# Optimization experiments

Hardware: AMD Instinct MI355X
Metric: run time of the kernel (lower is better)

The kernel has to match this reference:

```python
import jax, jax.numpy as jnp
import numpy as np

T, B, I, H = 1024, 256, 128, 256

def setup_inputs() -> dict:
    key = jax.random.key(0)
    k1, k2, k3, k4, k5 = jax.random.split(key, 5)
    x = jax.random.normal(k1, (T, B, I), dtype=jnp.float32)
    # nn.Linear default init: U(-1/sqrt(fan_in), 1/sqrt(fan_in))
    sW = 1.0 / np.sqrt(I)
    sV = 1.0 / np.sqrt(H)
    W = jax.random.uniform(k2, (H, I), minval=-sW, maxval=sW, dtype=jnp.float32)
    b_W = jax.random.uniform(k3, (H,), minval=-sW, maxval=sW, dtype=jnp.float32)
    V = jax.random.uniform(k4, (H, H), minval=-sV, maxval=sV, dtype=jnp.float32)
    b_V = jax.random.uniform(k5, (H,), minval=-sV, maxval=sV, dtype=jnp.float32)
    return {"x": x, "W": W, "b_W": b_W, "V": V, "b_V": b_V}

def reference(x, W, b_W, V, b_V):
    # x: (T, B, I). Hidden is always initialized to zeros (as in the torch code).
    # Precompute input projection for all timesteps (same math, one big GEMM).
    xW = jnp.einsum('tbi,hi->tbh', x, W) + b_W  # (T, B, H)
    h0 = jnp.zeros((x.shape[1], V.shape[0]), dtype=x.dtype)

    def step(h, xw_t):
        h_new = jnp.tanh(xw_t + h @ V.T + b_V)
        return h_new, h_new

    h_final, h_seq = jax.lax.scan(step, h0, xW)
    return h_seq, h_final
```

## Files before the change

### kernel.cpp

```cpp
#include <hip/hip_runtime.h>
#include <hip/hip_fp16.h>

#define TT 1024
#define BB 256
#define II 128
#define HH 256

typedef _Float16 f16x8 __attribute__((ext_vector_type(8)));
typedef _Float16 h2    __attribute__((ext_vector_type(2)));
typedef float    f32x4 __attribute__((ext_vector_type(4)));

union HU { h2 h; unsigned u; };
static __device__ __forceinline__ h2 as_h2(unsigned v) { HU t; t.u = v; return t.h; }
static __device__ __forceinline__ unsigned pack2f(float a, float b)
{
    HU t; t.h = h2{(_Float16)a, (_Float16)b}; return t.u;
}
static __device__ __forceinline__ float fdot2u(unsigned a, unsigned b, float c)
{
    return __builtin_amdgcn_fdot2(as_h2(a), as_h2(b), c, false);
}

#define LDS_BARRIER()                                            \
    do {                                                         \
        asm volatile("s_waitcnt lgkmcnt(0)" ::: "memory");       \
        __builtin_amdgcn_s_barrier();                            \
        __builtin_amdgcn_sched_barrier(0);                       \
    } while (0)

__device__ __forceinline__ float fast_tanh(float a)
{
    float e = __builtin_amdgcn_exp2f(a * 2.8853900817779268f);
    return 1.0f - 2.0f * __builtin_amdgcn_rcpf(e + 1.0f);
}

static __device__ __forceinline__ f16x8 cvt8(const float* p)
{
    float4 a = *(const float4*)p;
    float4 b = *(const float4*)(p + 4);
    f16x8 r;
    r[0]=(_Float16)a.x; r[1]=(_Float16)a.y; r[2]=(_Float16)a.z; r[3]=(_Float16)a.w;
    r[4]=(_Float16)b.x; r[5]=(_Float16)b.y; r[6]=(_Float16)b.z; r[7]=(_Float16)b.w;
    return r;
}

__global__ __launch_bounds__(256, 1)
void xw_gemm(const float* __restrict__ x, const float* __restrict__ W,
             const float* __restrict__ bW, const float* __restrict__ bV,
             float* __restrict__ xw)
{
    __shared__ _Float16 Wl[HH * II];
    const int tid  = threadIdx.x;
    const int l    = tid & 63;
    const int wv   = (__builtin_amdgcn_readfirstlane(tid) >> 6) & 3;
    const int lr   = l & 15;
    const int kgrp = l >> 4;

    {
        const int row = tid;
        const float4* src = (const float4*)(W + (size_t)row * II);
        unsigned* dst = (unsigned*)Wl;
        const int sw = (row & 7) << 4;
#pragma unroll
        for (int q = 0; q < II / 4; ++q) {
            float4 v = src[q];
            dst[(row * 256 + ((q * 8) ^ sw)) >> 2]     = pack2f(v.x, v.y);
            dst[(row * 256 + ((q * 8 + 4) ^ sw)) >> 2] = pack2f(v.z, v.w);
        }
    }
    __syncthreads();

    const size_t Mbase = (size_t)blockIdx.x * 64;
    const size_t arow  = Mbase + 16 * wv + lr;

    f16x8 afr[4];
#pragma unroll
    for (int kc = 0; kc < 4; ++kc)
        afr[kc] = cvt8(x + arow * II + kc * 32 + kgrp * 8);

    f32x4 acc[16];
#pragma unroll
    for (int nt = 0; nt < 16; ++nt) acc[nt] = f32x4{0.f, 0.f, 0.f, 0.f};

#pragma unroll
    for (int nt = 0; nt < 16; ++nt) {
        const int col = nt * 16 + lr;
        const int sw  = (col & 7) << 4;
#pragma unroll
        for (int kc = 0; kc < 4; ++kc) {
            f16x8 bfr = *(const f16x8*)((const char*)Wl + col * 256 +
                                        ((kc * 64 + kgrp * 16) ^ sw));
            acc[nt] = __builtin_amdgcn_mfma_f32_16x16x32_f16(afr[kc], bfr, acc[nt], 0, 0, 0);
        }
    }
#pragma unroll
    for (int nt = 0; nt < 16; ++nt) {
        const float bias = bW[nt * 16 + lr] + bV[nt * 16 + lr];
#pragma unroll
        for (int r = 0; r < 4; ++r) {
            size_t row = Mbase + 16 * wv + kgrp * 4 + r;
            xw[row * HH + nt * 16 + lr] = acc[nt][r] + bias;
        }
    }
}

__global__ __launch_bounds__(512, 2)
void rnn_v(const float* __restrict__ V, float* __restrict__ out)
{
    const int b   = blockIdx.x;
    const int tid = threadIdx.x;
    const int l   = tid & 63;
    const int w   = (__builtin_amdgcn_readfirstlane(tid) >> 6) & 7;
    const int lb  = 8 * w;

    __shared__ __align__(16) _Float16 hbuf[2][HH];
    __shared__ __align__(16) float    pbuf[8][HH];

    unsigned Vreg[4][16];
#pragma unroll
    for (int c = 0; c < 4; ++c) {
        const int j = 4 * l + c;
        const float* vr = V + (size_t)j * HH + 32 * w;
#pragma unroll
        for (int m = 0; m < 16; ++m) Vreg[c][m] = pack2f(vr[2 * m], vr[2 * m + 1]);
    }

    if (tid < HH) { hbuf[0][tid] = (_Float16)0.f; hbuf[1][tid] = (_Float16)0.f; }
    __syncthreads();

    float* __restrict__ seq = out;
    float* __restrict__ fin = out + (size_t)TT * BB * HH;

    float XA = 0.f, XB = 0.f;
    if (tid < HH) {
        XA = seq[((size_t)0 * BB + b) * HH + tid];
        XB = seq[((size_t)1 * BB + b) * HH + tid];
    }

#define RSTEP(P, X, T)                                                          \
    {                                                                           \
        uint2 hv = *(const uint2*)&hbuf[P][4 * l];             \
        float va[4][2] = {{0.f,0.f},{0.f,0.f},{0.f,0.f},{0.f,0.f}};             \
        _Pragma("unroll")                                                       \
        for (int i2 = 0; i2 < 8; ++i2) {                                        \
            unsigned s0 = (unsigned)__builtin_amdgcn_readlane((int)hv.x, lb + i2); \
            unsigned s1 = (unsigned)__builtin_amdgcn_readlane((int)hv.y, lb + i2); \
            _Pragma("unroll")                                                   \
            for (int c = 0; c < 4; ++c) {                                       \
                va[c][0] = fdot2u(s0, Vreg[c][2 * i2],     va[c][0]);           \
                va[c][1] = fdot2u(s1, Vreg[c][2 * i2 + 1], va[c][1]);           \
            }                                                                   \
        }                                                                       \
        f32x4 tot;                                                              \
        tot[0] = va[0][0] + va[0][1];                                           \
        tot[1] = va[1][0] + va[1][1];                                           \
        tot[2] = va[2][0] + va[2][1];                                           \
        tot[3] = va[3][0] + va[3][1];                                           \
        *(f32x4*)&pbuf[w][4 * l] = tot;                                         \
        LDS_BARRIER();                                        \
        if (tid < HH) {                                                         \
            float p0 = pbuf[0][tid], p1 = pbuf[1][tid];                         \
            float p2 = pbuf[2][tid], p3 = pbuf[3][tid];                         \
            float p4 = pbuf[4][tid], p5 = pbuf[5][tid];                         \
            float p6 = pbuf[6][tid], p7 = pbuf[7][tid];                         \
            float r  = (((p0 + p1) + (p2 + p3)) + ((p4 + p5) + (p6 + p7))) + X; \
            float hf = fast_tanh(r);                                            \
            seq[((size_t)(T) * BB + b) * HH + tid] = hf;                        \
            hbuf[(P) ^ 1][tid] = (_Float16)hf;                                  \
            if ((T) == TT - 1) fin[(size_t)b * HH + tid] = hf;                  \
            const int tp = ((T) + 2 < TT) ? (T) + 2 : (TT - 1);                 \
            X = seq[((size_t)tp * BB + b) * HH + tid];                          \
        }                                                                       \
        LDS_BARRIER();                                        \
    }

#pragma unroll 1
    for (int t = 0; t < TT; t += 2) {
        RSTEP(0, XA, t);
        RSTEP(1, XB, t + 1);
    }
#undef RSTEP
}

extern "C" void kernel_launch(void* const* d_in, const int* in_sizes, int n_in,
                              void* d_out, int out_size, void* d_ws, size_t ws_size,
                              hipStream_t stream)
{
    const float* x  = (const float*)d_in[0];
    const float* W  = (const float*)d_in[1];
    const float* bW = (const float*)d_in[2];
    const float* V  = (const float*)d_in[3];
    const float* bV = (const float*)d_in[4];
    float* out = (float*)d_out;

    xw_gemm<<<dim3((TT * BB) / 64), dim3(256), 0, stream>>>(x, W, bW, bV, out);
    rnn_v<<<dim3(BB), dim3(512), 0, stream>>>(V, out);
}
```

Baseline: 776.5 us.

## Use packed fp16 FMA accumulation and spread tanh epilogue across all waves

The recurrent matvec now accumulates in packed half precision with elementwise fma on h2 vectors instead of fdot2 with fp32 accumulators. Partial sums are converted to fp32 only for the cross-wave reduction. The per-step finalize (reduction, tanh, stores) moves from the first 256 threads (4 waves) to the first 32 lanes of each of the 8 waves, so the serial epilogue is shared by every wave. The fp16 accumulation increases rounding error in the recurrence, and the half-active waves use lanes less efficiently.

Result: slower. 858.2 us (+10.5%).

```diff
diff --git a/kernel.cpp b/kernel.cpp
--- a/kernel.cpp
+++ b/kernel.cpp
@@ -15,10 +15,6 @@
 static __device__ __forceinline__ unsigned pack2f(float a, float b)
 {
     HU t; t.h = h2{(_Float16)a, (_Float16)b}; return t.u;
-}
-static __device__ __forceinline__ float fdot2u(unsigned a, unsigned b, float c)
-{
-    return __builtin_amdgcn_fdot2(as_h2(a), as_h2(b), c, false);
 }
 
 #define LDS_BARRIER()                                            \
@@ -105,24 +101,27 @@
 }
 
 __global__ __launch_bounds__(512, 2)
-void rnn_v(const float* __restrict__ V, float* __restrict__ out)
+void rnn_v2(const float* __restrict__ V, float* __restrict__ out)
 {
     const int b   = blockIdx.x;
     const int tid = threadIdx.x;
     const int l   = tid & 63;
     const int w   = (__builtin_amdgcn_readfirstlane(tid) >> 6) & 7;
     const int lb  = 8 * w;
+    const int fo  = 32 * w + (l & 31);
+    const bool fact = (l < 32);
 
     __shared__ __align__(16) _Float16 hbuf[2][HH];
     __shared__ __align__(16) float    pbuf[8][HH];
 
-    unsigned Vreg[4][16];
+    h2 Vh[4][16];
 #pragma unroll
     for (int c = 0; c < 4; ++c) {
         const int j = 4 * l + c;
         const float* vr = V + (size_t)j * HH + 32 * w;
 #pragma unroll
-        for (int m = 0; m < 16; ++m) Vreg[c][m] = pack2f(vr[2 * m], vr[2 * m + 1]);
+        for (int m = 0; m < 16; ++m)
+            Vh[c][m] = h2{(_Float16)vr[2 * m], (_Float16)vr[2 * m + 1]};
     }
 
     if (tid < HH) { hbuf[0][tid] = (_Float16)0.f; hbuf[1][tid] = (_Float16)0.f; }
@@ -132,44 +131,48 @@
     float* __restrict__ fin = out + (size_t)TT * BB * HH;
 
     float XA = 0.f, XB = 0.f;
-    if (tid < HH) {
-        XA = seq[((size_t)0 * BB + b) * HH + tid];
-        XB = seq[((size_t)1 * BB + b) * HH + tid];
+    if (fact) {
+        XA = seq[((size_t)0 * BB + b) * HH + fo];
+        XB = seq[((size_t)1 * BB + b) * HH + fo];
     }
 
 #define RSTEP(P, X, T)                                                          \
     {                                                                           \
         uint2 hv = *(const uint2*)&hbuf[P][4 * l];             \
-        float va[4][2] = {{0.f,0.f},{0.f,0.f},{0.f,0.f},{0.f,0.f}};             \
+        h2 a0[4], a1[4];                                                        \
+        _Pragma("unroll")                                                       \
+        for (int c = 0; c < 4; ++c) { a0[c] = h2{0, 0}; a1[c] = h2{0, 0}; }     \
         _Pragma("unroll")                                                       \
         for (int i2 = 0; i2 < 8; ++i2) {                                        \
             unsigned s0 = (unsigned)__builtin_amdgcn_readlane((int)hv.x, lb + i2); \
             unsigned s1 = (unsigned)__builtin_amdgcn_readlane((int)hv.y, lb + i2); \
+            h2 b0 = as_h2(s0), b1 = as_h2(s1);                                  \
             _Pragma("unroll")                                                   \
             for (int c = 0; c < 4; ++c) {                                       \
-                va[c][0] = fdot2u(s0, Vreg[c][2 * i2],     va[c][0]);           \
-                va[c][1] = fdot2u(s1, Vreg[c][2 * i2 + 1], va[c][1]);           \
+                a0[c] = __builtin_elementwise_fma(b0, Vh[c][2 * i2],     a0[c]); \
+                a1[c] = __builtin_elementwise_fma(b1, Vh[c][2 * i2 + 1], a1[c]); \
             }                                                                   \
         }                                                                       \
         f32x4 tot;                                                              \
-        tot[0] = va[0][0] + va[0][1];                                           \
-        tot[1] = va[1][0] + va[1][1];                                           \
-        tot[2] = va[2][0] + va[2][1];                                           \
-        tot[3] = va[3][0] + va[3][1];                                           \
+        _Pragma("unroll")                                                       \
+        for (int c = 0; c < 4; ++c) {                                           \
+            h2 s = a0[c] + a1[c];                                               \
+            tot[c] = (float)s[0] + (float)s[1];                                 \
+        }                                                                       \
         *(f32x4*)&pbuf[w][4 * l] = tot;                                         \
         LDS_BARRIER();                                        \
-        if (tid < HH) {                                                         \
-            float p0 = pbuf[0][tid], p1 = pbuf[1][tid];                         \
-            float p2 = pbuf[2][tid], p3 = pbuf[3][tid];                         \
-            float p4 = pbuf[4][tid], p5 = pbuf[5][tid];                         \
-            float p6 = pbuf[6][tid], p7 = pbuf[7][tid];                         \
+        if (fact) {                                                             \
+            float p0 = pbuf[0][fo], p1 = pbuf[1][fo];                           \
+            float p2 = pbuf[2][fo], p3 = pbuf[3][fo];                           \
+            float p4 = pbuf[4][fo], p5 = pbuf[5][fo];                           \
+            float p6 = pbuf[6][fo], p7 = pbuf[7][fo];                           \
             float r  = (((p0 + p1) + (p2 + p3)) + ((p4 + p5) + (p6 + p7))) + X; \
             float hf = fast_tanh(r);                                            \
-            seq[((size_t)(T) * BB + b) * HH + tid] = hf;                        \
-            hbuf[(P) ^ 1][tid] = (_Float16)hf;                                  \
-            if ((T) == TT - 1) fin[(size_t)b * HH + tid] = hf;                  \
+            hbuf[(P) ^ 1][fo] = (_Float16)hf;                                   \
+            seq[((size_t)(T) * BB + b) * HH + fo] = hf;                         \
+            if ((T) == TT - 1) fin[(size_t)b * HH + fo] = hf;                   \
             const int tp = ((T) + 2 < TT) ? (T) + 2 : (TT - 1);                 \
-            X = seq[((size_t)tp * BB + b) * HH + tid];                          \
+            X = seq[((size_t)tp * BB + b) * HH + fo];                           \
         }                                                                       \
         LDS_BARRIER();                                        \
     }
@@ -194,5 +197,5 @@
     float* out = (float*)d_out;
 
     xw_gemm<<<dim3((TT * BB) / 64), dim3(256), 0, stream>>>(x, W, bW, bV, out);
-    rnn_v<<<dim3(BB), dim3(512), 0, stream>>>(V, out);
-}
+    rnn_v2<<<dim3(BB), dim3(512), 0, stream>>>(V, out);
+}
```
